# Kernel optimization log

Measured on AMD Instinct MI355X. Metric: run time of the kernel, lower is better.

## Reference

```python
import jax, jax.numpy as jnp
import numpy as np

TEMPERATURE = 1.0  # forward default
INIT_STD = 0.01    # per-class gate init: N(0, 0.01)

def setup_inputs() -> dict:
    key = jax.random.key(0)
    kf, kws, kw1, kw2 = jax.random.split(key, 4)
    B, F, H, C, E = 256, 2048, 512, 512, 8
    Hh = H // 2  # 256
    features = jax.random.normal(kf, (B, F), dtype=jnp.float32)
    # shared transform Linear(F, H) -- default torch init approximated by small normal
    Ws = jax.random.normal(kws, (F, H), dtype=jnp.float32) * (1.0 / np.sqrt(F))
    bs = jnp.zeros((H,), dtype=jnp.float32)
    # per-class gates, stacked over class dim: N(0, 0.01) init, zero bias (as in module)
    W1 = jax.random.normal(kw1, (C, H, Hh), dtype=jnp.float32) * INIT_STD
    b1 = jnp.zeros((C, Hh), dtype=jnp.float32)
    W2 = jax.random.normal(kw2, (C, Hh, E), dtype=jnp.float32) * INIT_STD
    b2 = jnp.zeros((C, E), dtype=jnp.float32)
    return {"features": features, "Ws": Ws, "bs": bs, "W1": W1, "b1": b1, "W2": W2, "b2": b2}

def reference(features, Ws, bs, W1, b1, W2, b2):
    # shared transform: Linear -> ReLU (Dropout is identity at inference)
    shared = jax.nn.relu(features @ Ws + bs)                      # [B, H]
    # batched per-class MLP: one grouped GEMM across all classes
    h = jax.nn.relu(jnp.einsum('bh,chk->bck', shared, W1) + b1)   # [B, C, H/2]
    gate_logits = jnp.einsum('bck,cke->bce', h, W2) + b2          # [B, C, E]
    gate_weights = jax.nn.softmax(gate_logits / TEMPERATURE, axis=-1)
    return (gate_weights, gate_logits)
```

## Files before the change

kernel.cpp:

```cpp
#include <hip/hip_runtime.h>
#include <hip/hip_bf16.h>

#define BATCH 256
#define F_DIM 2048
#define H_DIM 512
#define HH    256
#define NCLS  512
#define E_DIM 8

typedef __attribute__((ext_vector_type(8))) short  bf16x8;
typedef __attribute__((ext_vector_type(4))) float  f32x4;
typedef __attribute__((ext_vector_type(4))) unsigned short u16x4;

__device__ __forceinline__ unsigned short f2bf(float x) {
    union { float f; unsigned int u; } v; v.f = x;
    unsigned int r = v.u + 0x7fffu + ((v.u >> 16) & 1u);
    return (unsigned short)(r >> 16);
}

__global__ __launch_bounds__(256) void k_transpose(
    const float* __restrict__ Ws, unsigned short* __restrict__ WsT)
{
    __shared__ float tile[64][68];
    const int bid = blockIdx.x;
    const int kt = bid & 31;
    const int nt = bid >> 5;
    const int k0 = kt * 64, n0 = nt * 64;
    const int tx = threadIdx.x & 15, ty = threadIdx.x >> 4;

#pragma unroll
    for (int i = 0; i < 4; ++i) {
        const int row = ty + i * 16;
        f32x4 v = *(const f32x4*)(Ws + (size_t)(k0 + row) * H_DIM + n0 + tx * 4);
        *(f32x4*)(&tile[row][tx * 4]) = v;
    }
    __syncthreads();
#pragma unroll
    for (int i = 0; i < 4; ++i) {
        const int n = ty + i * 16;
        u16x4 o;
#pragma unroll
        for (int j = 0; j < 4; ++j) o[j] = f2bf(tile[tx * 4 + j][n]);
        *(u16x4*)(WsT + (size_t)(n0 + n) * F_DIM + k0 + tx * 4) = o;
    }
}

__global__ __launch_bounds__(256) void k_gemm1(
    const float* __restrict__ features,
    const unsigned short* __restrict__ WsT,
    float* __restrict__ partials)
{
    const int tid = threadIdx.x;
    const int lane = tid & 63;
    const int wave = tid >> 6;
    const int job = blockIdx.x * 4 + wave;
    const int kidx = job & 3;
    const int nt = (job >> 2) & 7;
    const int mt = job >> 5;
    const int l15 = lane & 15, quad = lane >> 4;
    const int m0 = mt * 16, n0 = nt * 64, kb = kidx * 512;

    f32x4 z = {0.f, 0.f, 0.f, 0.f};
    f32x4 acc[4];
#pragma unroll
    for (int nf = 0; nf < 4; ++nf) acc[nf] = z;

    for (int ks = 0; ks < 16; ++ks) {
        const int kk = kb + ks * 32 + quad * 8;
        f32x4 a0 = *(const f32x4*)(features + (size_t)(m0 + l15) * F_DIM + kk);
        f32x4 a1 = *(const f32x4*)(features + (size_t)(m0 + l15) * F_DIM + kk + 4);
        bf16x8 aF;
#pragma unroll
        for (int j = 0; j < 4; ++j) { aF[j] = (short)f2bf(a0[j]); aF[4 + j] = (short)f2bf(a1[j]); }
#pragma unroll
        for (int nf = 0; nf < 4; ++nf) {
            bf16x8 bF = *(const bf16x8*)(WsT + (size_t)(n0 + nf * 16 + l15) * F_DIM + kk);
            acc[nf] = __builtin_amdgcn_mfma_f32_16x16x32_bf16(aF, bF, acc[nf], 0, 0, 0);
        }
    }
    float* po = partials + (size_t)kidx * (BATCH * H_DIM);
#pragma unroll
    for (int nf = 0; nf < 4; ++nf)
#pragma unroll
        for (int r = 0; r < 4; ++r)
            po[(size_t)(m0 + quad * 4 + r) * H_DIM + n0 + nf * 16 + l15] = acc[nf][r];
}

__global__ __launch_bounds__(256) void k_reduce_relu(
    const float* __restrict__ partials, const float* __restrict__ bs,
    unsigned short* __restrict__ sharedA)
{
    const int idx = (blockIdx.x * 256 + threadIdx.x) * 4;
    f32x4 s = *(const f32x4*)(partials + idx);
    s += *(const f32x4*)(partials + BATCH * H_DIM + idx);
    s += *(const f32x4*)(partials + 2 * BATCH * H_DIM + idx);
    s += *(const f32x4*)(partials + 3 * BATCH * H_DIM + idx);
    s += *(const f32x4*)(bs + (idx & (H_DIM - 1)));
    u16x4 o;
#pragma unroll
    for (int j = 0; j < 4; ++j) {
        float v = s[j] > 0.f ? s[j] : 0.f;
        o[j] = f2bf(v);
    }
    *(u16x4*)(sharedA + idx) = o;
}

__global__ __launch_bounds__(256, 2) void k_main(
    const unsigned short* __restrict__ sharedA,
    const float* __restrict__ W1,
    const float* __restrict__ b1,
    const float* __restrict__ W2,
    const float* __restrict__ b2,
    float* __restrict__ out)
{
    const int c = blockIdx.x;
    const int tid = threadIdx.x;
    const int lane = tid & 63;
    const int wave = tid >> 6;
    const int l15 = lane & 15;
    const int quad = lane >> 4;
    const int m0 = wave * 64;
    const int nloc = tid & 127;
    const int half = tid >> 7;

    __shared__ unsigned short Blds[8 * 128 * 8];
    __shared__ float w2s[128 * 8];
    __shared__ float b1s[128];
    __shared__ float logits_s[BATCH * E_DIM];

    const float* W1c = W1 + (size_t)c * (H_DIM * HH);

    for (int pass = 0; pass < 2; ++pass) {
        const int n0p = pass * 128;
        {
            f32x4 w = *(const f32x4*)(W2 + (size_t)c * (HH * E_DIM) + n0p * E_DIM + tid * 4);
            *(f32x4*)(w2s + tid * 4) = w;
            if (tid < 128) b1s[tid] = b1[(size_t)c * HH + n0p + tid];
        }
        f32x4 z = {0.f, 0.f, 0.f, 0.f};
        f32x4 acc[4][8];
#pragma unroll
        for (int mf = 0; mf < 4; ++mf)
#pragma unroll
            for (int nf = 0; nf < 8; ++nf) acc[mf][nf] = z;

        float rg[32];
#pragma unroll
        for (int i = 0; i < 4; ++i)
#pragma unroll
            for (int j = 0; j < 8; ++j)
                rg[i * 8 + j] = W1c[(size_t)((half + 2 * i) * 8 + j) * HH + n0p + nloc];

        for (int ch = 0; ch < 8; ++ch) {
#pragma unroll
            for (int i = 0; i < 4; ++i) {
                bf16x8 v;
#pragma unroll
                for (int j = 0; j < 8; ++j) v[j] = (short)rg[i * 8 + j] * 0 + (short)f2bf(rg[i * 8 + j]);
                *(bf16x8*)(&Blds[(((half + 2 * i) * 128 + nloc)) * 8]) = v;
            }
            __syncthreads();

            float rn[32];
            if (ch < 7) {
#pragma unroll
                for (int i = 0; i < 4; ++i)
#pragma unroll
                    for (int j = 0; j < 8; ++j)
                        rn[i * 8 + j] = W1c[(size_t)((ch + 1) * 64 + (half + 2 * i) * 8 + j) * HH + n0p + nloc];
            }

#pragma unroll
            for (int ks = 0; ks < 2; ++ks) {
                const int kglob = ch * 64 + ks * 32 + quad * 8;
                bf16x8 aF[4];
#pragma unroll
                for (int mf = 0; mf < 4; ++mf)
                    aF[mf] = *(const bf16x8*)(sharedA + (size_t)(m0 + mf * 16 + l15) * H_DIM + kglob);
#pragma unroll
                for (int nf = 0; nf < 8; ++nf) {
                    bf16x8 bF = *(const bf16x8*)(&Blds[((ks * 4 + quad) * 128 + nf * 16 + l15) * 8]);
#pragma unroll
                    for (int mf = 0; mf < 4; ++mf)
                        acc[mf][nf] = __builtin_amdgcn_mfma_f32_16x16x32_bf16(aF[mf], bF, acc[mf][nf], 0, 0, 0);
                }
            }
            __syncthreads();
#pragma unroll
            for (int q = 0; q < 32; ++q) rg[q] = rn[q];
        }

#pragma unroll
        for (int mf = 0; mf < 4; ++mf) {
            float part[4][E_DIM];
#pragma unroll
            for (int r = 0; r < 4; ++r)
#pragma unroll
                for (int e = 0; e < E_DIM; ++e) part[r][e] = 0.f;
#pragma unroll
            for (int nf = 0; nf < 8; ++nf) {
                const int col = nf * 16 + l15;
                f32x4 wA = *(const f32x4*)(w2s + col * 8);
                f32x4 wB = *(const f32x4*)(w2s + col * 8 + 4);
                const float bb = b1s[col];
#pragma unroll
                for (int r = 0; r < 4; ++r) {
                    float h = acc[mf][nf][r] + bb;
                    h = h > 0.f ? h : 0.f;
                    part[r][0] += h * wA[0]; part[r][1] += h * wA[1];
                    part[r][2] += h * wA[2]; part[r][3] += h * wA[3];
                    part[r][4] += h * wB[0]; part[r][5] += h * wB[1];
                    part[r][6] += h * wB[2]; part[r][7] += h * wB[3];
                }
            }
#pragma unroll
            for (int r = 0; r < 4; ++r)
#pragma unroll
                for (int e = 0; e < E_DIM; ++e) {
                    float v = part[r][e];
                    v += __shfl_xor(v, 1, 16);
                    v += __shfl_xor(v, 2, 16);
                    v += __shfl_xor(v, 4, 16);
                    v += __shfl_xor(v, 8, 16);
                    part[r][e] = v;
                }
            if (l15 == 0) {
#pragma unroll
                for (int r = 0; r < 4; ++r) {
                    const int row = m0 + mf * 16 + quad * 4 + r;
                    f32x4 lo = {part[r][0], part[r][1], part[r][2], part[r][3]};
                    f32x4 hi = {part[r][4], part[r][5], part[r][6], part[r][7]};
                    if (pass == 0) {
                        *(f32x4*)(logits_s + row * 8) = lo;
                        *(f32x4*)(logits_s + row * 8 + 4) = hi;
                    } else {
                        *(f32x4*)(logits_s + row * 8) = *(f32x4*)(logits_s + row * 8) + lo;
                        *(f32x4*)(logits_s + row * 8 + 4) = *(f32x4*)(logits_s + row * 8 + 4) + hi;
                    }
                }
            }
        }
        __syncthreads();
    }

    f32x4 lg0 = *(f32x4*)(logits_s + tid * 8);
    f32x4 lg1 = *(f32x4*)(logits_s + tid * 8 + 4);
    lg0 += *(const f32x4*)(b2 + (size_t)c * E_DIM);
    lg1 += *(const f32x4*)(b2 + (size_t)c * E_DIM + 4);

    float lg[8] = {lg0[0], lg0[1], lg0[2], lg0[3], lg1[0], lg1[1], lg1[2], lg1[3]};
    float mx = lg[0];
#pragma unroll
    for (int e = 1; e < 8; ++e) mx = lg[e] > mx ? lg[e] : mx;
    float ex[8], s = 0.f;
#pragma unroll
    for (int e = 0; e < 8; ++e) { ex[e] = __expf(lg[e] - mx); s += ex[e]; }
    const float inv = 1.f / s;

    const size_t ob = ((size_t)tid * NCLS + c) * E_DIM;
    f32x4 w0 = {ex[0] * inv, ex[1] * inv, ex[2] * inv, ex[3] * inv};
    f32x4 w1 = {ex[4] * inv, ex[5] * inv, ex[6] * inv, ex[7] * inv};
    *(f32x4*)(out + ob) = w0;
    *(f32x4*)(out + ob + 4) = w1;
    const size_t lbase = (size_t)BATCH * NCLS * E_DIM;
    f32x4 o0 = {lg[0], lg[1], lg[2], lg[3]};
    f32x4 o1 = {lg[4], lg[5], lg[6], lg[7]};
    *(f32x4*)(out + lbase + ob) = o0;
    *(f32x4*)(out + lbase + ob + 4) = o1;
}

extern "C" void kernel_launch(void* const* d_in, const int* in_sizes, int n_in,
                              void* d_out, int out_size, void* d_ws, size_t ws_size,
                              hipStream_t stream) {
    const float* features = (const float*)d_in[0];
    const float* Ws       = (const float*)d_in[1];
    const float* bs       = (const float*)d_in[2];
    const float* W1       = (const float*)d_in[3];
    const float* b1       = (const float*)d_in[4];
    const float* W2       = (const float*)d_in[5];
    const float* b2       = (const float*)d_in[6];
    float* out = (float*)d_out;

    char* ws = (char*)d_ws;
    unsigned short* WsT     = (unsigned short*)ws;
    float*          parts   = (float*)(ws + 2097152);
    unsigned short* sharedA = (unsigned short*)(ws + 4194304);

    hipLaunchKernelGGL(k_transpose,   dim3(256), dim3(256), 0, stream, Ws, WsT);
    hipLaunchKernelGGL(k_gemm1,       dim3(128), dim3(256), 0, stream, features, WsT, parts);
    hipLaunchKernelGGL(k_reduce_relu, dim3(128), dim3(256), 0, stream, parts, bs, sharedA);
    hipLaunchKernelGGL(k_main,        dim3(NCLS), dim3(256), 0, stream, sharedA, W1, b1, W2, b2, out);
}
```

Before: 447.0 us.

## Drop Ws transpose, widen split-K for GEMM1, restructure main kernel without LDS staging

Removes the separate Ws transpose kernel; GEMM1 now reads fp32 Ws directly with strided loads and converts to bf16 in registers, using 8-way split-K over 256 blocks. The main per-class kernel moves to 512 threads with 8 waves, each owning a 64-column by 128-row tile. W1 fragments are loaded straight from global into double-buffered registers instead of being staged through LDS, and the per-wave partial logits are reduced through shared slots. This cuts a launch and the LDS barriers but adds uncoalesced column-strided global loads and higher register pressure.

Measured after the change: 471.4 us. 5.5% more time.

```diff
diff --git a/kernel.cpp b/kernel.cpp
--- a/kernel.cpp
+++ b/kernel.cpp
@@ -18,54 +18,28 @@
     return (unsigned short)(r >> 16);
 }
 
-__global__ __launch_bounds__(256) void k_transpose(
-    const float* __restrict__ Ws, unsigned short* __restrict__ WsT)
-{
-    __shared__ float tile[64][68];
-    const int bid = blockIdx.x;
-    const int kt = bid & 31;
-    const int nt = bid >> 5;
-    const int k0 = kt * 64, n0 = nt * 64;
-    const int tx = threadIdx.x & 15, ty = threadIdx.x >> 4;
-
-#pragma unroll
-    for (int i = 0; i < 4; ++i) {
-        const int row = ty + i * 16;
-        f32x4 v = *(const f32x4*)(Ws + (size_t)(k0 + row) * H_DIM + n0 + tx * 4);
-        *(f32x4*)(&tile[row][tx * 4]) = v;
-    }
-    __syncthreads();
-#pragma unroll
-    for (int i = 0; i < 4; ++i) {
-        const int n = ty + i * 16;
-        u16x4 o;
-#pragma unroll
-        for (int j = 0; j < 4; ++j) o[j] = f2bf(tile[tx * 4 + j][n]);
-        *(u16x4*)(WsT + (size_t)(n0 + n) * F_DIM + k0 + tx * 4) = o;
-    }
-}
-
 __global__ __launch_bounds__(256) void k_gemm1(
     const float* __restrict__ features,
-    const unsigned short* __restrict__ WsT,
+    const float* __restrict__ Ws,
     float* __restrict__ partials)
 {
     const int tid = threadIdx.x;
     const int lane = tid & 63;
     const int wave = tid >> 6;
     const int job = blockIdx.x * 4 + wave;
-    const int kidx = job & 3;
-    const int nt = (job >> 2) & 7;
-    const int mt = job >> 5;
+    const int kidx = job & 7;
+    const int ng  = (job >> 3) & 7;
+    const int mt  = job >> 6;
     const int l15 = lane & 15, quad = lane >> 4;
-    const int m0 = mt * 16, n0 = nt * 64, kb = kidx * 512;
+    const int m0 = mt * 16, n0 = ng * 64, kb = kidx * 256;
 
     f32x4 z = {0.f, 0.f, 0.f, 0.f};
     f32x4 acc[4];
 #pragma unroll
     for (int nf = 0; nf < 4; ++nf) acc[nf] = z;
 
-    for (int ks = 0; ks < 16; ++ks) {
+#pragma unroll
+    for (int ks = 0; ks < 8; ++ks) {
         const int kk = kb + ks * 32 + quad * 8;
         f32x4 a0 = *(const f32x4*)(features + (size_t)(m0 + l15) * F_DIM + kk);
         f32x4 a1 = *(const f32x4*)(features + (size_t)(m0 + l15) * F_DIM + kk + 4);
@@ -74,7 +48,10 @@
         for (int j = 0; j < 4; ++j) { aF[j] = (short)f2bf(a0[j]); aF[4 + j] = (short)f2bf(a1[j]); }
 #pragma unroll
         for (int nf = 0; nf < 4; ++nf) {
-            bf16x8 bF = *(const bf16x8*)(WsT + (size_t)(n0 + nf * 16 + l15) * F_DIM + kk);
+            bf16x8 bF;
+#pragma unroll
+            for (int j = 0; j < 8; ++j)
+                bF[j] = (short)f2bf(Ws[(size_t)(kk + j) * H_DIM + n0 + nf * 16 + l15]);
             acc[nf] = __builtin_amdgcn_mfma_f32_16x16x32_bf16(aF, bF, acc[nf], 0, 0, 0);
         }
     }
@@ -92,9 +69,9 @@
 {
     const int idx = (blockIdx.x * 256 + threadIdx.x) * 4;
     f32x4 s = *(const f32x4*)(partials + idx);
-    s += *(const f32x4*)(partials + BATCH * H_DIM + idx);
-    s += *(const f32x4*)(partials + 2 * BATCH * H_DIM + idx);
-    s += *(const f32x4*)(partials + 3 * BATCH * H_DIM + idx);
+#pragma unroll
+    for (int p = 1; p < 8; ++p)
+        s += *(const f32x4*)(partials + (size_t)p * (BATCH * H_DIM) + idx);
     s += *(const f32x4*)(bs + (idx & (H_DIM - 1)));
     u16x4 o;
 #pragma unroll
@@ -105,7 +82,7 @@
     *(u16x4*)(sharedA + idx) = o;
 }
 
-__global__ __launch_bounds__(256, 2) void k_main(
+__global__ __launch_bounds__(512) void k_main(
     const unsigned short* __restrict__ sharedA,
     const float* __restrict__ W1,
     const float* __restrict__ b1,
@@ -119,154 +96,142 @@
     const int wave = tid >> 6;
     const int l15 = lane & 15;
     const int quad = lane >> 4;
-    const int m0 = wave * 64;
-    const int nloc = tid & 127;
-    const int half = tid >> 7;
-
-    __shared__ unsigned short Blds[8 * 128 * 8];
-    __shared__ float w2s[128 * 8];
-    __shared__ float b1s[128];
-    __shared__ float logits_s[BATCH * E_DIM];
-
-    const float* W1c = W1 + (size_t)c * (H_DIM * HH);
-
-    for (int pass = 0; pass < 2; ++pass) {
-        const int n0p = pass * 128;
-        {
-            f32x4 w = *(const f32x4*)(W2 + (size_t)c * (HH * E_DIM) + n0p * E_DIM + tid * 4);
-            *(f32x4*)(w2s + tid * 4) = w;
-            if (tid < 128) b1s[tid] = b1[(size_t)c * HH + n0p + tid];
-        }
-        f32x4 z = {0.f, 0.f, 0.f, 0.f};
-        f32x4 acc[4][8];
-#pragma unroll
-        for (int mf = 0; mf < 4; ++mf)
-#pragma unroll
-            for (int nf = 0; nf < 8; ++nf) acc[mf][nf] = z;
-
-        float rg[32];
-#pragma unroll
-        for (int i = 0; i < 4; ++i)
+    const int g  = wave & 3;
+    const int mh = wave >> 2;
+    const int n0w = g * 64;
+    const int m0w = mh * 128;
+
+    const float* __restrict__ W1c = W1 + (size_t)c * (H_DIM * HH);
+
+    __shared__ float slot[4][BATCH][E_DIM];
+
+    f32x4 z = {0.f, 0.f, 0.f, 0.f};
+    f32x4 acc[8][4];
+#pragma unroll
+    for (int mf = 0; mf < 8; ++mf)
+#pragma unroll
+        for (int nf = 0; nf < 4; ++nf) acc[mf][nf] = z;
+
+    float braw[2][32];
+#pragma unroll
+    for (int nf = 0; nf < 4; ++nf)
+#pragma unroll
+        for (int j = 0; j < 8; ++j)
+            braw[0][nf * 8 + j] = W1c[(size_t)(quad * 8 + j) * HH + n0w + nf * 16 + l15];
+
+#pragma unroll
+    for (int ks = 0; ks < 16; ++ks) {
+        const int cur = ks & 1;
+        if (ks < 15) {
+            const int k0n = (ks + 1) * 32;
+#pragma unroll
+            for (int nf = 0; nf < 4; ++nf)
+#pragma unroll
+                for (int j = 0; j < 8; ++j)
+                    braw[cur ^ 1][nf * 8 + j] =
+                        W1c[(size_t)(k0n + quad * 8 + j) * HH + n0w + nf * 16 + l15];
+        }
+        bf16x8 bF[4];
+#pragma unroll
+        for (int nf = 0; nf < 4; ++nf)
 #pragma unroll
             for (int j = 0; j < 8; ++j)
-                rg[i * 8 + j] = W1c[(size_t)((half + 2 * i) * 8 + j) * HH + n0p + nloc];
-
-        for (int ch = 0; ch < 8; ++ch) {
-#pragma unroll
-            for (int i = 0; i < 4; ++i) {
-                bf16x8 v;
-#pragma unroll
-                for (int j = 0; j < 8; ++j) v[j] = (short)rg[i * 8 + j] * 0 + (short)f2bf(rg[i * 8 + j]);
-                *(bf16x8*)(&Blds[(((half + 2 * i) * 128 + nloc)) * 8]) = v;
+                bF[nf][j] = (short)f2bf(braw[cur][nf * 8 + j]);
+
+        const int k0 = ks * 32 + quad * 8;
+#pragma unroll
+        for (int mf = 0; mf < 8; ++mf) {
+            bf16x8 aF = *(const bf16x8*)(sharedA + (size_t)(m0w + mf * 16 + l15) * H_DIM + k0);
+#pragma unroll
+            for (int nf = 0; nf < 4; ++nf)
+                acc[mf][nf] = __builtin_amdgcn_mfma_f32_16x16x32_bf16(aF, bF[nf], acc[mf][nf], 0, 0, 0);
+        }
+    }
+
+    float b1v[4];
+    f32x4 w2a[4], w2b[4];
+#pragma unroll
+    for (int nf = 0; nf < 4; ++nf) {
+        const int col = n0w + nf * 16 + l15;
+        b1v[nf] = b1[(size_t)c * HH + col];
+        w2a[nf] = *(const f32x4*)(W2 + ((size_t)c * HH + col) * E_DIM);
+        w2b[nf] = *(const f32x4*)(W2 + ((size_t)c * HH + col) * E_DIM + 4);
+    }
+
+#pragma unroll
+    for (int mf = 0; mf < 8; ++mf) {
+        float part[4][E_DIM];
+#pragma unroll
+        for (int r = 0; r < 4; ++r)
+#pragma unroll
+            for (int e = 0; e < E_DIM; ++e) part[r][e] = 0.f;
+#pragma unroll
+        for (int nf = 0; nf < 4; ++nf) {
+#pragma unroll
+            for (int r = 0; r < 4; ++r) {
+                float h = acc[mf][nf][r] + b1v[nf];
+                h = h > 0.f ? h : 0.f;
+                part[r][0] += h * w2a[nf][0]; part[r][1] += h * w2a[nf][1];
+                part[r][2] += h * w2a[nf][2]; part[r][3] += h * w2a[nf][3];
+                part[r][4] += h * w2b[nf][0]; part[r][5] += h * w2b[nf][1];
+                part[r][6] += h * w2b[nf][2]; part[r][7] += h * w2b[nf][3];
             }
-            __syncthreads();
-
-            float rn[32];
-            if (ch < 7) {
-#pragma unroll
-                for (int i = 0; i < 4; ++i)
-#pragma unroll
-                    for (int j = 0; j < 8; ++j)
-                        rn[i * 8 + j] = W1c[(size_t)((ch + 1) * 64 + (half + 2 * i) * 8 + j) * HH + n0p + nloc];
+        }
+#pragma unroll
+        for (int r = 0; r < 4; ++r)
+#pragma unroll
+            for (int e = 0; e < E_DIM; ++e) {
+                float v = part[r][e];
+                v += __shfl_xor(v, 1, 16);
+                v += __shfl_xor(v, 2, 16);
+                v += __shfl_xor(v, 4, 16);
+                v += __shfl_xor(v, 8, 16);
+                part[r][e] = v;
             }
-
-#pragma unroll
-            for (int ks = 0; ks < 2; ++ks) {
-                const int kglob = ch * 64 + ks * 32 + quad * 8;
-                bf16x8 aF[4];
-#pragma unroll
-                for (int mf = 0; mf < 4; ++mf)
-                    aF[mf] = *(const bf16x8*)(sharedA + (size_t)(m0 + mf * 16 + l15) * H_DIM + kglob);
-#pragma unroll
-                for (int nf = 0; nf < 8; ++nf) {
-                    bf16x8 bF = *(const bf16x8*)(&Blds[((ks * 4 + quad) * 128 + nf * 16 + l15) * 8]);
-#pragma unroll
-                    for (int mf = 0; mf < 4; ++mf)
-                        acc[mf][nf] = __builtin_amdgcn_mfma_f32_16x16x32_bf16(aF[mf], bF, acc[mf][nf], 0, 0, 0);
-                }
+        if (l15 == 0) {
+#pragma unroll
+            for (int r = 0; r < 4; ++r) {
+                const int row = m0w + mf * 16 + quad * 4 + r;
+                f32x4 lo = {part[r][0], part[r][1], part[r][2], part[r][3]};
+                f32x4 hi = {part[r][4], part[r][5], part[r][6], part[r][7]};
+                *(f32x4*)(&slot[g][row][0]) = lo;
+                *(f32x4*)(&slot[g][row][4]) = hi;
             }
-            __syncthreads();
-#pragma unroll
-            for (int q = 0; q < 32; ++q) rg[q] = rn[q];
-        }
-
-#pragma unroll
-        for (int mf = 0; mf < 4; ++mf) {
-            float part[4][E_DIM];
-#pragma unroll
-            for (int r = 0; r < 4; ++r)
-#pragma unroll
-                for (int e = 0; e < E_DIM; ++e) part[r][e] = 0.f;
-#pragma unroll
-            for (int nf = 0; nf < 8; ++nf) {
-                const int col = nf * 16 + l15;
-                f32x4 wA = *(const f32x4*)(w2s + col * 8);
-                f32x4 wB = *(const f32x4*)(w2s + col * 8 + 4);
-                const float bb = b1s[col];
-#pragma unroll
-                for (int r = 0; r < 4; ++r) {
-                    float h = acc[mf][nf][r] + bb;
-                    h = h > 0.f ? h : 0.f;
-                    part[r][0] += h * wA[0]; part[r][1] += h * wA[1];
-                    part[r][2] += h * wA[2]; part[r][3] += h * wA[3];
-                    part[r][4] += h * wB[0]; part[r][5] += h * wB[1];
-                    part[r][6] += h * wB[2]; part[r][7] += h * wB[3];
-                }
-            }
-#pragma unroll
-            for (int r = 0; r < 4; ++r)
-#pragma unroll
-                for (int e = 0; e < E_DIM; ++e) {
-                    float v = part[r][e];
-                    v += __shfl_xor(v, 1, 16);
-                    v += __shfl_xor(v, 2, 16);
-                    v += __shfl_xor(v, 4, 16);
-                    v += __shfl_xor(v, 8, 16);
-                    part[r][e] = v;
-                }
-            if (l15 == 0) {
-#pragma unroll
-                for (int r = 0; r < 4; ++r) {
-                    const int row = m0 + mf * 16 + quad * 4 + r;
-                    f32x4 lo = {part[r][0], part[r][1], part[r][2], part[r][3]};
-                    f32x4 hi = {part[r][4], part[r][5], part[r][6], part[r][7]};
-                    if (pass == 0) {
-                        *(f32x4*)(logits_s + row * 8) = lo;
-                        *(f32x4*)(logits_s + row * 8 + 4) = hi;
-                    } else {
-                        *(f32x4*)(logits_s + row * 8) = *(f32x4*)(logits_s + row * 8) + lo;
-                        *(f32x4*)(logits_s + row * 8 + 4) = *(f32x4*)(logits_s + row * 8 + 4) + hi;
-                    }
-                }
-            }
-        }
-        __syncthreads();
-    }
-
-    f32x4 lg0 = *(f32x4*)(logits_s + tid * 8);
-    f32x4 lg1 = *(f32x4*)(logits_s + tid * 8 + 4);
-    lg0 += *(const f32x4*)(b2 + (size_t)c * E_DIM);
-    lg1 += *(const f32x4*)(b2 + (size_t)c * E_DIM + 4);
-
-    float lg[8] = {lg0[0], lg0[1], lg0[2], lg0[3], lg1[0], lg1[1], lg1[2], lg1[3]};
-    float mx = lg[0];
-#pragma unroll
-    for (int e = 1; e < 8; ++e) mx = lg[e] > mx ? lg[e] : mx;
-    float ex[8], s = 0.f;
-#pragma unroll
-    for (int e = 0; e < 8; ++e) { ex[e] = __expf(lg[e] - mx); s += ex[e]; }
-    const float inv = 1.f / s;
-
-    const size_t ob = ((size_t)tid * NCLS + c) * E_DIM;
-    f32x4 w0 = {ex[0] * inv, ex[1] * inv, ex[2] * inv, ex[3] * inv};
-    f32x4 w1 = {ex[4] * inv, ex[5] * inv, ex[6] * inv, ex[7] * inv};
-    *(f32x4*)(out + ob) = w0;
-    *(f32x4*)(out + ob + 4) = w1;
-    const size_t lbase = (size_t)BATCH * NCLS * E_DIM;
-    f32x4 o0 = {lg[0], lg[1], lg[2], lg[3]};
-    f32x4 o1 = {lg[4], lg[5], lg[6], lg[7]};
-    *(f32x4*)(out + lbase + ob) = o0;
-    *(f32x4*)(out + lbase + ob + 4) = o1;
+        }
+    }
+    __syncthreads();
+
+    if (tid < BATCH) {
+        f32x4 lg0 = *(f32x4*)(&slot[0][tid][0]);
+        f32x4 lg1 = *(f32x4*)(&slot[0][tid][4]);
+#pragma unroll
+        for (int s = 1; s < 4; ++s) {
+            lg0 += *(f32x4*)(&slot[s][tid][0]);
+            lg1 += *(f32x4*)(&slot[s][tid][4]);
+        }
+        lg0 += *(const f32x4*)(b2 + (size_t)c * E_DIM);
+        lg1 += *(const f32x4*)(b2 + (size_t)c * E_DIM + 4);
+
+        float lg[8] = {lg0[0], lg0[1], lg0[2], lg0[3], lg1[0], lg1[1], lg1[2], lg1[3]};
+        float mx = lg[0];
+#pragma unroll
+        for (int e = 1; e < 8; ++e) mx = lg[e] > mx ? lg[e] : mx;
+        float ex[8], s = 0.f;
+#pragma unroll
+        for (int e = 0; e < 8; ++e) { ex[e] = __expf(lg[e] - mx); s += ex[e]; }
+        const float inv = 1.f / s;
+
+        const size_t ob = ((size_t)tid * NCLS + c) * E_DIM;
+        f32x4 w0 = {ex[0] * inv, ex[1] * inv, ex[2] * inv, ex[3] * inv};
+        f32x4 w1 = {ex[4] * inv, ex[5] * inv, ex[6] * inv, ex[7] * inv};
+        *(f32x4*)(out + ob) = w0;
+        *(f32x4*)(out + ob + 4) = w1;
+        const size_t lbase = (size_t)BATCH * NCLS * E_DIM;
+        f32x4 o0 = {lg[0], lg[1], lg[2], lg[3]};
+        f32x4 o1 = {lg[4], lg[5], lg[6], lg[7]};
+        *(f32x4*)(out + lbase + ob) = o0;
+        *(f32x4*)(out + lbase + ob + 4) = o1;
+    }
 }
 
 extern "C" void kernel_launch(void* const* d_in, const int* in_sizes, int n_in,
@@ -282,12 +247,10 @@
     float* out = (float*)d_out;
 
     char* ws = (char*)d_ws;
-    unsigned short* WsT     = (unsigned short*)ws;
-    float*          parts   = (float*)(ws + 2097152);
-    unsigned short* sharedA = (unsigned short*)(ws + 4194304);
-
-    hipLaunchKernelGGL(k_transpose,   dim3(256), dim3(256), 0, stream, Ws, WsT);
-    hipLaunchKernelGGL(k_gemm1,       dim3(128), dim3(256), 0, stream, features, WsT, parts);
+    float*          parts   = (float*)ws;
+    unsigned short* sharedA = (unsigned short*)(ws + 4 * 1048576);
+
+    hipLaunchKernelGGL(k_gemm1,       dim3(256), dim3(256), 0, stream, features, Ws, parts);
     hipLaunchKernelGGL(k_reduce_relu, dim3(128), dim3(256), 0, stream, parts, bs, sharedA);
-    hipLaunchKernelGGL(k_main,        dim3(NCLS), dim3(256), 0, stream, sharedA, W1, b1, W2, b2, out);
-}
+    hipLaunchKernelGGL(k_main,        dim3(NCLS), dim3(512), 0, stream, sharedA, W1, b1, W2, b2, out);
+}
```
